# Performance work log

Hardware: AMD Instinct MI355X
Metric: run time of the kernel (lower is better)

Reference implementation:

```python
import jax, jax.numpy as jnp
import numpy as np

B, S, D_IN, D_H, H = 4, 2048, 512, 512, 8
HD = D_H // H
EPS = 1e-5


def setup_inputs() -> dict:
    key = jax.random.key(0)
    ks = jax.random.split(key, 12)
    s = lambda d: 1.0 / np.sqrt(d)
    return {
        "x": jax.random.normal(ks[0], (B, S, D_IN), jnp.float32),
        "mask": jnp.ones((B, S, S), jnp.int32),
        "Wq": jax.random.normal(ks[1], (D_IN, D_H), jnp.float32) * s(D_IN),
        "bq": jnp.zeros((D_H,), jnp.float32),
        "Wk": jax.random.normal(ks[2], (D_IN, D_H), jnp.float32) * s(D_IN),
        "bk": jnp.zeros((D_H,), jnp.float32),
        "Wv": jax.random.normal(ks[3], (D_IN, D_H), jnp.float32) * s(D_IN),
        "bv": jnp.zeros((D_H,), jnp.float32),
        "pos_enc": jax.random.normal(ks[4], (S, D_H), jnp.float32),
        "Wo": jax.random.normal(ks[5], (D_H, D_H), jnp.float32) * s(D_H),
        "bo": jnp.zeros((D_H,), jnp.float32),
        "gamma": jnp.ones((D_H,), jnp.float32),
        "beta": jnp.zeros((D_H,), jnp.float32),
    }


def reference(x, mask, Wq, bq, Wk, bk, Wv, bv, pos_enc, Wo, bo, gamma, beta):
    b, s, _ = x.shape
    pe = pos_enc[:s][None]  # [1,S,Dh]
    q = x @ Wq + bq + pe
    k = x @ Wk + bk + pe
    v = x @ Wv + bv
    # [B,H,S,hd]
    q = q.reshape(b, s, H, HD).transpose(0, 2, 1, 3)
    k = k.reshape(b, s, H, HD).transpose(0, 2, 1, 3)
    v = v.reshape(b, s, H, HD).transpose(0, 2, 1, 3)
    scores = jnp.einsum("bhqd,bhkd->bhqk", q, k) / np.sqrt(HD).astype(np.float32)
    scores = jnp.where(mask[:, None] == 0, -jnp.inf, scores)
    attn = jax.nn.softmax(scores, axis=-1)  # dropout is identity in eval mode
    out = jnp.einsum("bhqk,bhkd->bhqd", attn, v)
    out = out.transpose(0, 2, 1, 3).reshape(b, s, D_H)
    out = out @ Wo + bo
    mu = out.mean(-1, keepdims=True)
    var = out.var(-1, keepdims=True)
    out = (out - mu) / jnp.sqrt(var + EPS) * gamma + beta
    return out, attn
```

## Files before the change

kernel.cpp:

```cpp
#include <hip/hip_runtime.h>
#include <hip/hip_bf16.h>

typedef __attribute__((ext_vector_type(8))) __bf16 bf16x8;
typedef __attribute__((ext_vector_type(8))) unsigned short u16x8;
typedef __attribute__((ext_vector_type(4))) float f32x4;
typedef __attribute__((ext_vector_type(4))) int i32x4;
typedef __attribute__((ext_vector_type(4))) unsigned int u32x4;

#define NB 4
#define NS 2048
#define NH 8
#define NHD 64
#define NDH 512

__device__ __forceinline__ unsigned short f2bf(float f) {
  union { float f; unsigned int u; } v; v.f = f;
  unsigned int r = v.u + 0x7FFFu + ((v.u >> 16) & 1u);
  return (unsigned short)(r >> 16);
}

__device__ __forceinline__ f32x4 MFMA(u16x8 a, u16x8 b, f32x4 c) {
  return __builtin_amdgcn_mfma_f32_16x16x32_bf16(
      __builtin_bit_cast(bf16x8, a), __builtin_bit_cast(bf16x8, b), c, 0, 0, 0);
}

__global__ __launch_bounds__(256) void prep_kernel(
    const float* __restrict__ x, const int* __restrict__ mask,
    const float* __restrict__ Wq, const float* __restrict__ Wk,
    const float* __restrict__ Wv, const float* __restrict__ Wo,
    unsigned short* __restrict__ xb, unsigned short* __restrict__ Wt,
    unsigned int* __restrict__ mb) {
  const int bid = blockIdx.x, t = threadIdx.x;
  if (bid < 2048) {
    size_t base = ((size_t)bid * 256 + t) * 8;
    f32x4 a = *(const f32x4*)(x + base);
    f32x4 b = *(const f32x4*)(x + base + 4);
    u16x8 o;
    o[0] = f2bf(a[0]); o[1] = f2bf(a[1]); o[2] = f2bf(a[2]); o[3] = f2bf(a[3]);
    o[4] = f2bf(b[0]); o[5] = f2bf(b[1]); o[6] = f2bf(b[2]); o[7] = f2bf(b[3]);
    *(u16x8*)(xb + base) = o;
  } else if (bid < 3072) {
    __shared__ float lds[32][33];
    int wb = bid - 2048;
    int mat = wb >> 8, tile = wb & 255, tr = tile >> 4, tc = tile & 15;
    const float* W = (mat == 0) ? Wq : (mat == 1) ? Wk : (mat == 2) ? Wv : Wo;
    int col = t & 31, rbase = t >> 5;
    for (int i = 0; i < 4; ++i) {
      int row = rbase + i * 8;
      lds[row][col] = W[(size_t)(tr * 32 + row) * 512 + tc * 32 + col];
    }
    __syncthreads();
    for (int i = 0; i < 4; ++i) {
      int row = rbase + i * 8;
      Wt[((size_t)(mat * 512 + tc * 32 + row)) * 512 + tr * 32 + col] =
          f2bf(lds[col][row]);
    }
  } else {
    int widx = (bid - 3072) * 256 + t;
    const int* mp = mask + (size_t)widx * 32;
    unsigned int word = 0;
    for (int i = 0; i < 8; ++i) {
      i32x4 m = *(const i32x4*)(mp + i * 4);
      word |= (m[0] != 0 ? 1u : 0u) << (i * 4);
      word |= (m[1] != 0 ? 1u : 0u) << (i * 4 + 1);
      word |= (m[2] != 0 ? 1u : 0u) << (i * 4 + 2);
      word |= (m[3] != 0 ? 1u : 0u) << (i * 4 + 3);
    }
    mb[widx] = word;
  }
}

__global__ __launch_bounds__(256) void gemm_kernel(
    const unsigned short* __restrict__ A, const unsigned short* __restrict__ Bt,
    int mode, unsigned short* __restrict__ qb, unsigned short* __restrict__ kb,
    unsigned short* __restrict__ vb, const float* __restrict__ bq,
    const float* __restrict__ bk, const float* __restrict__ bv,
    const float* __restrict__ pe, float* __restrict__ proj,
    const float* __restrict__ bo) {
  const int t = threadIdx.x;
  const int w = t >> 6, lane = t & 63, l15 = lane & 15, quad = lane >> 4;
  const int n0 = blockIdx.x * 64, m0 = blockIdx.y * 64;
  __shared__ unsigned short a_lds[64 * 40];
  __shared__ unsigned short b_lds[64 * 40];
  f32x4 acc[4] = {};
  const int srow = t >> 2, sc8 = (t & 3) * 8;
  for (int k0 = 0; k0 < 512; k0 += 32) {
    u16x8 av = *(const u16x8*)(A + (size_t)(m0 + srow) * 512 + k0 + sc8);
    u16x8 bvv = *(const u16x8*)(Bt + (size_t)(n0 + srow) * 512 + k0 + sc8);
    __syncthreads();
    *(u16x8*)(a_lds + srow * 40 + sc8) = av;
    *(u16x8*)(b_lds + srow * 40 + sc8) = bvv;
    __syncthreads();
    u16x8 af = *(const u16x8*)(a_lds + (16 * w + l15) * 40 + quad * 8);
    for (int nt = 0; nt < 4; ++nt) {
      u16x8 bf_ = *(const u16x8*)(b_lds + (nt * 16 + l15) * 40 + quad * 8);
      acc[nt] = MFMA(af, bf_, acc[nt]);
    }
  }
  if (mode == 0) {
    for (int nt = 0; nt < 4; ++nt) {
      int j = n0 + nt * 16 + l15;
      int sel = j >> 9, jj = j & 511;
      int h = jj >> 6, hd = jj & 63;
      float bias = (sel == 0) ? bq[jj] : (sel == 1) ? bk[jj] : bv[jj];
      unsigned short* dst = (sel == 0) ? qb : (sel == 1) ? kb : vb;
      for (int r = 0; r < 4; ++r) {
        int m = m0 + 16 * w + quad * 4 + r;
        int bb = m >> 11, s = m & 2047;
        float v = acc[nt][r] + bias;
        if (sel < 2) v += pe[(size_t)s * 512 + jj];
        dst[(((size_t)bb * NH + h) * NS + s) * NHD + hd] = f2bf(v);
      }
    }
  } else {
    for (int nt = 0; nt < 4; ++nt) {
      int j = n0 + nt * 16 + l15;
      float bias = bo[j];
      for (int r = 0; r < 4; ++r) {
        int m = m0 + 16 * w + quad * 4 + r;
        proj[(size_t)m * 512 + j] = acc[nt][r] + bias;
      }
    }
  }
}

__global__ __launch_bounds__(256) void vtrans_kernel(
    const unsigned short* __restrict__ v, unsigned short* __restrict__ vT) {
  const int bh = blockIdx.y, st = blockIdx.x, t = threadIdx.x;
  const int s0 = st * 64;
  __shared__ unsigned int ldsT[64 * 36];
  int sp = t & 31, c8 = t >> 5;
  const unsigned short* vp = v + ((size_t)bh * NS + s0 + 2 * sp) * NHD + c8 * 8;
  u16x8 a = *(const u16x8*)(vp);
  u16x8 b = *(const u16x8*)(vp + NHD);
  for (int i = 0; i < 8; ++i) {
    unsigned int word = (unsigned int)a[i] | ((unsigned int)b[i] << 16);
    ldsT[(c8 * 8 + i) * 36 + sp] = word;
  }
  __syncthreads();
  int hd = t >> 2, cc = t & 3;
  u32x4 w0 = *(const u32x4*)(ldsT + hd * 36 + cc * 8);
  u32x4 w1 = *(const u32x4*)(ldsT + hd * 36 + cc * 8 + 4);
  unsigned short* op = vT + ((size_t)bh * NHD + hd) * NS + s0 + cc * 16;
  *(u32x4*)(op) = w0;
  *(u32x4*)(op + 8) = w1;
}

__global__ __launch_bounds__(256) void attn_kernel(
    const unsigned short* __restrict__ qg, const unsigned short* __restrict__ kg,
    const unsigned short* __restrict__ vTg, const unsigned int* __restrict__ mb,
    float* __restrict__ attnp_base, unsigned short* __restrict__ ao) {
  const int qt = blockIdx.x, bh = blockIdx.y;
  const int bb = bh >> 3, hh = bh & 7;
  const int t = threadIdx.x, w = t >> 6, lane = t & 63;
  const int l15 = lane & 15, quad = lane >> 4;
  const int sq0 = qt * 64;

  __shared__ unsigned short q_lds[64 * 72];
  __shared__ unsigned short k_lds[64 * 72];
  __shared__ unsigned short vt_lds[64 * 72];
  __shared__ float p_lds[64 * 68];

  const unsigned short* qptr = qg + ((size_t)bh * NS + sq0) * NHD;
  const unsigned short* kbase = kg + (size_t)bh * NS * NHD;
  const unsigned short* vtbase = vTg + (size_t)bh * NHD * NS;

  for (int it = 0; it < 2; ++it) {
    int idx = t + it * 256, r = idx >> 3, c8 = (idx & 7) * 8;
    *(u16x8*)(q_lds + r * 72 + c8) = *(const u16x8*)(qptr + r * 64 + c8);
  }
  __syncthreads();
  const u16x8 a0 = *(const u16x8*)(q_lds + (16 * w + l15) * 72 + quad * 8);
  const u16x8 a1 = *(const u16x8*)(q_lds + (16 * w + l15) * 72 + 32 + quad * 8);

  float mI[4], lI[4];
  for (int r = 0; r < 4; ++r) { mI[r] = -1e30f; lI[r] = 0.f; }
  const size_t mrow0 = ((size_t)bb * NS + sq0 + 16 * w + quad * 4) * 64;

  for (int kt = 0; kt < 32; ++kt) {
    for (int it = 0; it < 2; ++it) {
      int idx = t + it * 256, r = idx >> 3, c8 = (idx & 7) * 8;
      *(u16x8*)(k_lds + r * 72 + c8) =
          *(const u16x8*)(kbase + (size_t)(kt * 64 + r) * 64 + c8);
    }
    __syncthreads();
    f32x4 sc[4];
    for (int nt = 0; nt < 4; ++nt) {
      u16x8 b0 = *(const u16x8*)(k_lds + (nt * 16 + l15) * 72 + quad * 8);
      u16x8 b1 = *(const u16x8*)(k_lds + (nt * 16 + l15) * 72 + 32 + quad * 8);
      f32x4 acc = {0.f, 0.f, 0.f, 0.f};
      acc = MFMA(a0, b0, acc);
      acc = MFMA(a1, b1, acc);
      sc[nt] = acc;
    }
    unsigned int mw0[4], mw1[4];
    for (int r = 0; r < 4; ++r) {
      mw0[r] = mb[mrow0 + (size_t)r * 64 + kt * 2];
      mw1[r] = mb[mrow0 + (size_t)r * 64 + kt * 2 + 1];
    }
    float tmax[4] = {-1e30f, -1e30f, -1e30f, -1e30f};
    for (int nt = 0; nt < 4; ++nt) {
      int cl = nt * 16 + l15;
      for (int r = 0; r < 4; ++r) {
        float sv = sc[nt][r] * 0.125f;
        unsigned int wsel = (cl < 32) ? mw0[r] : mw1[r];
        if (!((wsel >> (cl & 31)) & 1u)) sv = -1e30f;
        sc[nt][r] = sv;
        tmax[r] = fmaxf(tmax[r], sv);
      }
    }
    for (int off = 1; off < 16; off <<= 1)
      for (int r = 0; r < 4; ++r)
        tmax[r] = fmaxf(tmax[r], __shfl_xor(tmax[r], off, 64));
    float mN[4], tsum[4] = {0.f, 0.f, 0.f, 0.f};
    for (int r = 0; r < 4; ++r) mN[r] = fmaxf(mI[r], tmax[r]);
    for (int nt = 0; nt < 4; ++nt)
      for (int r = 0; r < 4; ++r) tsum[r] += __expf(sc[nt][r] - mN[r]);
    for (int off = 1; off < 16; off <<= 1)
      for (int r = 0; r < 4; ++r) tsum[r] += __shfl_xor(tsum[r], off, 64);
    for (int r = 0; r < 4; ++r) {
      lI[r] = lI[r] * __expf(mI[r] - mN[r]) + tsum[r];
      mI[r] = mN[r];
    }
    __syncthreads();
  }

  float invl[4];
  for (int r = 0; r < 4; ++r) invl[r] = 1.0f / lI[r];
  float* attnp = attnp_base + ((size_t)bh * NS + sq0) * NS;
  f32x4 oacc[4] = {};

  for (int kt = 0; kt < 32; ++kt) {
    for (int it = 0; it < 4; ++it) {
      int idx = t + (it & 1) * 256, r = idx >> 3, c8 = (idx & 7) * 8;
      if (it < 2)
        *(u16x8*)(k_lds + r * 72 + c8) =
            *(const u16x8*)(kbase + (size_t)(kt * 64 + r) * 64 + c8);
      else
        *(u16x8*)(vt_lds + r * 72 + c8) =
            *(const u16x8*)(vtbase + (size_t)r * NS + kt * 64 + c8);
    }
    __syncthreads();
    f32x4 sc[4];
    for (int nt = 0; nt < 4; ++nt) {
      u16x8 b0 = *(const u16x8*)(k_lds + (nt * 16 + l15) * 72 + quad * 8);
      u16x8 b1 = *(const u16x8*)(k_lds + (nt * 16 + l15) * 72 + 32 + quad * 8);
      f32x4 acc = {0.f, 0.f, 0.f, 0.f};
      acc = MFMA(a0, b0, acc);
      acc = MFMA(a1, b1, acc);
      sc[nt] = acc;
    }
    unsigned int mw0[4], mw1[4];
    for (int r = 0; r < 4; ++r) {
      mw0[r] = mb[mrow0 + (size_t)r * 64 + kt * 2];
      mw1[r] = mb[mrow0 + (size_t)r * 64 + kt * 2 + 1];
    }
    for (int nt = 0; nt < 4; ++nt) {
      int cl = nt * 16 + l15;
      for (int r = 0; r < 4; ++r) {
        float sv = sc[nt][r] * 0.125f;
        unsigned int wsel = (cl < 32) ? mw0[r] : mw1[r];
        if (!((wsel >> (cl & 31)) & 1u)) sv = -1e30f;
        float pv = __expf(sv - mI[r]) * invl[r];
        attnp[(size_t)(16 * w + quad * 4 + r) * NS + kt * 64 + cl] = pv;
        p_lds[(16 * w + quad * 4 + r) * 68 + cl] = pv;
      }
    }
    __syncthreads();
    for (int kk = 0; kk < 64; kk += 32) {
      f32x4 pa0 = *(const f32x4*)(p_lds + (16 * w + l15) * 68 + kk + quad * 8);
      f32x4 pa1 = *(const f32x4*)(p_lds + (16 * w + l15) * 68 + kk + quad * 8 + 4);
      u16x8 af;
      af[0] = f2bf(pa0[0]); af[1] = f2bf(pa0[1]);
      af[2] = f2bf(pa0[2]); af[3] = f2bf(pa0[3]);
      af[4] = f2bf(pa1[0]); af[5] = f2bf(pa1[1]);
      af[6] = f2bf(pa1[2]); af[7] = f2bf(pa1[3]);
      for (int nto = 0; nto < 4; ++nto) {
        u16x8 bf_ = *(const u16x8*)(vt_lds + (nto * 16 + l15) * 72 + kk + quad * 8);
        oacc[nto] = MFMA(af, bf_, oacc[nto]);
      }
    }
    __syncthreads();
  }
  for (int nto = 0; nto < 4; ++nto)
    for (int r = 0; r < 4; ++r) {
      int s = sq0 + 16 * w + quad * 4 + r;
      ao[((size_t)(bb * NS + s)) * NDH + hh * 64 + nto * 16 + l15] =
          f2bf(oacc[nto][r]);
    }
}

__global__ __launch_bounds__(256) void ln_kernel(
    const float* __restrict__ proj, const float* __restrict__ gamma,
    const float* __restrict__ beta, float* __restrict__ out) {
  const int t = threadIdx.x, w = t >> 6, lane = t & 63;
  const int row = blockIdx.x * 4 + w;
  const float* pr = proj + (size_t)row * 512 + lane * 8;
  f32x4 v0 = *(const f32x4*)(pr);
  f32x4 v1 = *(const f32x4*)(pr + 4);
  float s = 0.f, s2 = 0.f;
  for (int j = 0; j < 4; ++j) {
    s += v0[j] + v1[j];
    s2 += v0[j] * v0[j] + v1[j] * v1[j];
  }
  for (int off = 1; off < 64; off <<= 1) {
    s += __shfl_xor(s, off, 64);
    s2 += __shfl_xor(s2, off, 64);
  }
  float mu = s * (1.f / 512.f);
  float var = s2 * (1.f / 512.f) - mu * mu;
  float rs = rsqrtf(var + 1e-5f);
  f32x4 g0 = *(const f32x4*)(gamma + lane * 8);
  f32x4 g1 = *(const f32x4*)(gamma + lane * 8 + 4);
  f32x4 be0 = *(const f32x4*)(beta + lane * 8);
  f32x4 be1 = *(const f32x4*)(beta + lane * 8 + 4);
  f32x4 o0, o1;
  for (int j = 0; j < 4; ++j) {
    o0[j] = (v0[j] - mu) * rs * g0[j] + be0[j];
    o1[j] = (v1[j] - mu) * rs * g1[j] + be1[j];
  }
  float* op = out + (size_t)row * 512 + lane * 8;
  *(f32x4*)(op) = o0;
  *(f32x4*)(op + 4) = o1;
}

extern "C" void kernel_launch(void* const* d_in, const int* in_sizes, int n_in,
                              void* d_out, int out_size, void* d_ws,
                              size_t ws_size, hipStream_t stream) {
  const float* x = (const float*)d_in[0];
  const int* mask = (const int*)d_in[1];
  const float* Wq = (const float*)d_in[2];
  const float* bq = (const float*)d_in[3];
  const float* Wk = (const float*)d_in[4];
  const float* bk = (const float*)d_in[5];
  const float* Wv = (const float*)d_in[6];
  const float* bv = (const float*)d_in[7];
  const float* pe = (const float*)d_in[8];
  const float* Wo = (const float*)d_in[9];
  const float* bo = (const float*)d_in[10];
  const float* gamma = (const float*)d_in[11];
  const float* beta = (const float*)d_in[12];
  float* out = (float*)d_out;

  char* p = (char*)d_ws;
  unsigned short* xb = (unsigned short*)p; p += (size_t)4194304 * 2;
  unsigned short* Wt = (unsigned short*)p; p += (size_t)2048 * 512 * 2;
  unsigned short* qb = (unsigned short*)p; p += (size_t)4194304 * 2;
  unsigned short* kb = (unsigned short*)p; p += (size_t)4194304 * 2;
  unsigned short* vb = (unsigned short*)p; p += (size_t)4194304 * 2;
  unsigned short* vT = (unsigned short*)p; p += (size_t)4194304 * 2;
  unsigned short* ao = (unsigned short*)p; p += (size_t)4194304 * 2;
  float* proj = (float*)p; p += (size_t)4194304 * 4;
  unsigned int* mb = (unsigned int*)p; p += (size_t)524288 * 4;

  prep_kernel<<<5120, 256, 0, stream>>>(x, mask, Wq, Wk, Wv, Wo, xb, Wt, mb);
  gemm_kernel<<<dim3(24, 128), 256, 0, stream>>>(xb, Wt, 0, qb, kb, vb, bq, bk,
                                                 bv, pe, nullptr, nullptr);
  vtrans_kernel<<<dim3(32, 32), 256, 0, stream>>>(vb, vT);
  attn_kernel<<<dim3(32, 32), 256, 0, stream>>>(qb, kb, vT, mb,
                                                out + 4194304, ao);
  gemm_kernel<<<dim3(8, 128), 256, 0, stream>>>(
      ao, Wt + (size_t)1536 * 512, 1, nullptr, nullptr, nullptr, nullptr,
      nullptr, nullptr, nullptr, proj, bo);
  ln_kernel<<<2048, 256, 0, stream>>>(proj, gamma, beta, out);
}
```

Baseline: 952.1 us.

## Make attention waves independent: direct global K/V fragments, per-wave bf16 P, deferred reductions

The attention kernel stops staging Q, K and V^T through shared memory with block-wide barriers. Each wave now loads its MFMA fragments straight from global memory (relying on cache), writes P as bf16 into a private per-wave LDS slice, and uses only compiler fences instead of __syncthreads. The row max/sum cross-lane shuffle reduction is moved out of the first pass and done once with a merge of (m,l) pairs, and launch bounds request 4 blocks per CU. The intent is to cut barrier stalls, LDS traffic and per-tile shuffles, at the cost of redundant, less coalesced global/L2 reads of K and V^T across waves.

Result: slower. 1.017 ms (+6.8%).

```diff
diff --git a/kernel.cpp b/kernel.cpp
--- a/kernel.cpp
+++ b/kernel.cpp
@@ -146,7 +146,7 @@
   *(u32x4*)(op + 8) = w1;
 }
 
-__global__ __launch_bounds__(256) void attn_kernel(
+__global__ __launch_bounds__(256, 4) void attn_kernel(
     const unsigned short* __restrict__ qg, const unsigned short* __restrict__ kg,
     const unsigned short* __restrict__ vTg, const unsigned int* __restrict__ mb,
     float* __restrict__ attnp_base, unsigned short* __restrict__ ao) {
@@ -156,133 +156,127 @@
   const int l15 = lane & 15, quad = lane >> 4;
   const int sq0 = qt * 64;
 
-  __shared__ unsigned short q_lds[64 * 72];
-  __shared__ unsigned short k_lds[64 * 72];
-  __shared__ unsigned short vt_lds[64 * 72];
-  __shared__ float p_lds[64 * 68];
-
-  const unsigned short* qptr = qg + ((size_t)bh * NS + sq0) * NHD;
+  __shared__ unsigned short p_lds[4][16 * 72];
+  unsigned short* pw = &p_lds[w][0];
+
+  const unsigned short* qptr = qg + ((size_t)bh * NS + sq0 + 16 * w) * NHD;
   const unsigned short* kbase = kg + (size_t)bh * NS * NHD;
   const unsigned short* vtbase = vTg + (size_t)bh * NHD * NS;
 
-  for (int it = 0; it < 2; ++it) {
-    int idx = t + it * 256, r = idx >> 3, c8 = (idx & 7) * 8;
-    *(u16x8*)(q_lds + r * 72 + c8) = *(const u16x8*)(qptr + r * 64 + c8);
-  }
-  __syncthreads();
-  const u16x8 a0 = *(const u16x8*)(q_lds + (16 * w + l15) * 72 + quad * 8);
-  const u16x8 a1 = *(const u16x8*)(q_lds + (16 * w + l15) * 72 + 32 + quad * 8);
+  const u16x8 a0 = *(const u16x8*)(qptr + l15 * 64 + quad * 8);
+  const u16x8 a1 = *(const u16x8*)(qptr + l15 * 64 + 32 + quad * 8);
 
   float mI[4], lI[4];
+#pragma unroll
   for (int r = 0; r < 4; ++r) { mI[r] = -1e30f; lI[r] = 0.f; }
   const size_t mrow0 = ((size_t)bb * NS + sq0 + 16 * w + quad * 4) * 64;
 
   for (int kt = 0; kt < 32; ++kt) {
-    for (int it = 0; it < 2; ++it) {
-      int idx = t + it * 256, r = idx >> 3, c8 = (idx & 7) * 8;
-      *(u16x8*)(k_lds + r * 72 + c8) =
-          *(const u16x8*)(kbase + (size_t)(kt * 64 + r) * 64 + c8);
-    }
-    __syncthreads();
+    const unsigned short* kp = kbase + (size_t)kt * 64 * NHD;
     f32x4 sc[4];
-    for (int nt = 0; nt < 4; ++nt) {
-      u16x8 b0 = *(const u16x8*)(k_lds + (nt * 16 + l15) * 72 + quad * 8);
-      u16x8 b1 = *(const u16x8*)(k_lds + (nt * 16 + l15) * 72 + 32 + quad * 8);
+#pragma unroll
+    for (int nt = 0; nt < 4; ++nt) {
+      u16x8 b0 = *(const u16x8*)(kp + (nt * 16 + l15) * 64 + quad * 8);
+      u16x8 b1 = *(const u16x8*)(kp + (nt * 16 + l15) * 64 + 32 + quad * 8);
       f32x4 acc = {0.f, 0.f, 0.f, 0.f};
       acc = MFMA(a0, b0, acc);
       acc = MFMA(a1, b1, acc);
       sc[nt] = acc;
     }
     unsigned int mw0[4], mw1[4];
+#pragma unroll
     for (int r = 0; r < 4; ++r) {
       mw0[r] = mb[mrow0 + (size_t)r * 64 + kt * 2];
       mw1[r] = mb[mrow0 + (size_t)r * 64 + kt * 2 + 1];
     }
-    float tmax[4] = {-1e30f, -1e30f, -1e30f, -1e30f};
+    float tm[4] = {-1e30f, -1e30f, -1e30f, -1e30f};
+#pragma unroll
     for (int nt = 0; nt < 4; ++nt) {
       int cl = nt * 16 + l15;
+#pragma unroll
       for (int r = 0; r < 4; ++r) {
         float sv = sc[nt][r] * 0.125f;
         unsigned int wsel = (cl < 32) ? mw0[r] : mw1[r];
         if (!((wsel >> (cl & 31)) & 1u)) sv = -1e30f;
         sc[nt][r] = sv;
-        tmax[r] = fmaxf(tmax[r], sv);
-      }
-    }
-    for (int off = 1; off < 16; off <<= 1)
-      for (int r = 0; r < 4; ++r)
-        tmax[r] = fmaxf(tmax[r], __shfl_xor(tmax[r], off, 64));
-    float mN[4], tsum[4] = {0.f, 0.f, 0.f, 0.f};
-    for (int r = 0; r < 4; ++r) mN[r] = fmaxf(mI[r], tmax[r]);
-    for (int nt = 0; nt < 4; ++nt)
-      for (int r = 0; r < 4; ++r) tsum[r] += __expf(sc[nt][r] - mN[r]);
-    for (int off = 1; off < 16; off <<= 1)
-      for (int r = 0; r < 4; ++r) tsum[r] += __shfl_xor(tsum[r], off, 64);
-    for (int r = 0; r < 4; ++r) {
-      lI[r] = lI[r] * __expf(mI[r] - mN[r]) + tsum[r];
-      mI[r] = mN[r];
-    }
-    __syncthreads();
-  }
-
+        tm[r] = fmaxf(tm[r], sv);
+      }
+    }
+#pragma unroll
+    for (int r = 0; r < 4; ++r) {
+      float mN = fmaxf(mI[r], tm[r]);
+      float sum = 0.f;
+#pragma unroll
+      for (int nt = 0; nt < 4; ++nt) sum += __expf(sc[nt][r] - mN);
+      lI[r] = lI[r] * __expf(mI[r] - mN) + sum;
+      mI[r] = mN;
+    }
+  }
+#pragma unroll
+  for (int off = 1; off < 16; off <<= 1) {
+#pragma unroll
+    for (int r = 0; r < 4; ++r) {
+      float mo = __shfl_xor(mI[r], off, 64);
+      float lo = __shfl_xor(lI[r], off, 64);
+      float mN = fmaxf(mI[r], mo);
+      lI[r] = lI[r] * __expf(mI[r] - mN) + lo * __expf(mo - mN);
+      mI[r] = mN;
+    }
+  }
   float invl[4];
+#pragma unroll
   for (int r = 0; r < 4; ++r) invl[r] = 1.0f / lI[r];
-  float* attnp = attnp_base + ((size_t)bh * NS + sq0) * NS;
+
+  float* attnp = attnp_base + ((size_t)bh * NS + sq0 + 16 * w) * NS;
   f32x4 oacc[4] = {};
 
   for (int kt = 0; kt < 32; ++kt) {
-    for (int it = 0; it < 4; ++it) {
-      int idx = t + (it & 1) * 256, r = idx >> 3, c8 = (idx & 7) * 8;
-      if (it < 2)
-        *(u16x8*)(k_lds + r * 72 + c8) =
-            *(const u16x8*)(kbase + (size_t)(kt * 64 + r) * 64 + c8);
-      else
-        *(u16x8*)(vt_lds + r * 72 + c8) =
-            *(const u16x8*)(vtbase + (size_t)r * NS + kt * 64 + c8);
-    }
-    __syncthreads();
+    const unsigned short* kp = kbase + (size_t)kt * 64 * NHD;
     f32x4 sc[4];
-    for (int nt = 0; nt < 4; ++nt) {
-      u16x8 b0 = *(const u16x8*)(k_lds + (nt * 16 + l15) * 72 + quad * 8);
-      u16x8 b1 = *(const u16x8*)(k_lds + (nt * 16 + l15) * 72 + 32 + quad * 8);
+#pragma unroll
+    for (int nt = 0; nt < 4; ++nt) {
+      u16x8 b0 = *(const u16x8*)(kp + (nt * 16 + l15) * 64 + quad * 8);
+      u16x8 b1 = *(const u16x8*)(kp + (nt * 16 + l15) * 64 + 32 + quad * 8);
       f32x4 acc = {0.f, 0.f, 0.f, 0.f};
       acc = MFMA(a0, b0, acc);
       acc = MFMA(a1, b1, acc);
       sc[nt] = acc;
     }
     unsigned int mw0[4], mw1[4];
+#pragma unroll
     for (int r = 0; r < 4; ++r) {
       mw0[r] = mb[mrow0 + (size_t)r * 64 + kt * 2];
       mw1[r] = mb[mrow0 + (size_t)r * 64 + kt * 2 + 1];
     }
+#pragma unroll
     for (int nt = 0; nt < 4; ++nt) {
       int cl = nt * 16 + l15;
+#pragma unroll
       for (int r = 0; r < 4; ++r) {
         float sv = sc[nt][r] * 0.125f;
         unsigned int wsel = (cl < 32) ? mw0[r] : mw1[r];
         if (!((wsel >> (cl & 31)) & 1u)) sv = -1e30f;
         float pv = __expf(sv - mI[r]) * invl[r];
-        attnp[(size_t)(16 * w + quad * 4 + r) * NS + kt * 64 + cl] = pv;
-        p_lds[(16 * w + quad * 4 + r) * 68 + cl] = pv;
-      }
-    }
-    __syncthreads();
+        attnp[(size_t)(quad * 4 + r) * NS + kt * 64 + cl] = pv;
+        pw[(quad * 4 + r) * 72 + cl] = f2bf(pv);
+      }
+    }
+    asm volatile("" ::: "memory");
+#pragma unroll
     for (int kk = 0; kk < 64; kk += 32) {
-      f32x4 pa0 = *(const f32x4*)(p_lds + (16 * w + l15) * 68 + kk + quad * 8);
-      f32x4 pa1 = *(const f32x4*)(p_lds + (16 * w + l15) * 68 + kk + quad * 8 + 4);
-      u16x8 af;
-      af[0] = f2bf(pa0[0]); af[1] = f2bf(pa0[1]);
-      af[2] = f2bf(pa0[2]); af[3] = f2bf(pa0[3]);
-      af[4] = f2bf(pa1[0]); af[5] = f2bf(pa1[1]);
-      af[6] = f2bf(pa1[2]); af[7] = f2bf(pa1[3]);
+      u16x8 af = *(const u16x8*)(pw + l15 * 72 + kk + quad * 8);
+#pragma unroll
       for (int nto = 0; nto < 4; ++nto) {
-        u16x8 bf_ = *(const u16x8*)(vt_lds + (nto * 16 + l15) * 72 + kk + quad * 8);
+        u16x8 bf_ = *(const u16x8*)(vtbase + (size_t)(nto * 16 + l15) * NS +
+                                    kt * 64 + kk + quad * 8);
         oacc[nto] = MFMA(af, bf_, oacc[nto]);
       }
     }
-    __syncthreads();
-  }
+    asm volatile("" ::: "memory");
+  }
+#pragma unroll
   for (int nto = 0; nto < 4; ++nto)
+#pragma unroll
     for (int r = 0; r < 4; ++r) {
       int s = sq0 + 16 * w + quad * 4 + r;
       ao[((size_t)(bb * NS + s)) * NDH + hh * 64 + nto * 16 + l15] =
```
